# Optimization experiments

Hardware: AMD Instinct MI355X
Metric: run time of the kernel (lower is better)

## Reference

```python
import jax, jax.numpy as jnp
import numpy as np

TEMPERATURE = 11.313708498984761  # sqrt(128)


def setup_inputs() -> dict:
    key = jax.random.key(0)
    kq, kk, kv = jax.random.split(key, 3)
    b, n, m, d, dv = 16, 2048, 2048, 128, 128
    return {
        "queries": jax.random.normal(kq, (b, n, d), dtype=jnp.float32),
        "keys": jax.random.normal(kk, (b, m, d), dtype=jnp.float32),
        "values": jax.random.normal(kv, (b, m, dv), dtype=jnp.float32),
    }


def reference(queries, keys, values):
    # scores: [b, n, m]
    scores = jnp.einsum('bnd,bmd->bnm', queries, keys) / TEMPERATURE
    attn = jax.nn.softmax(scores, axis=2)
    # out: [b, n, d']
    return jnp.einsum('bnm,bmd->bnd', attn, values)
```

## Files before the change

### kernel.cpp

```cpp
#include <hip/hip_runtime.h>


#define BATCH 16
#define SEQ   2048
#define DIM   128
#define NT    (SEQ / 64)

typedef short bf16x8 __attribute__((ext_vector_type(8)));
typedef float f32x16 __attribute__((ext_vector_type(16)));

static __device__ __forceinline__ unsigned pk2(float lo, float hi) {
  union { float f; unsigned u; } a, b;
  a.f = lo; b.f = hi;
  return ((b.u + 0x8000u) & 0xffff0000u) | ((a.u + 0x8000u) >> 16);
}
static __device__ __forceinline__ float fast_exp2(float x) {
#if __has_builtin(__builtin_amdgcn_exp2f)
  return __builtin_amdgcn_exp2f(x);
#else
  return exp2f(x);
#endif
}

typedef __attribute__((address_space(1))) const unsigned int g_u32;
typedef __attribute__((address_space(3))) unsigned int l_u32;
static __device__ __forceinline__ void gl2lds16(const unsigned short* g, unsigned short* l) {
  __builtin_amdgcn_global_load_lds((g_u32*)g, (l_u32*)l, 16, 0, 0);
}

__global__ __launch_bounds__(256)
void prep_kernel(const float* __restrict__ K, const float* __restrict__ V,
                 unsigned short* __restrict__ Kb, unsigned short* __restrict__ Vt,
                 float scale) {
  const int bx = blockIdx.x, tid = threadIdx.x;
  if (bx < 2048) {
    size_t idx = (size_t)bx * 256 + tid;
    const float4* kf = (const float4*)K;
    float4 a = kf[idx * 2], c = kf[idx * 2 + 1];
    uint4 o;
    o.x = pk2(a.x * scale, a.y * scale);
    o.y = pk2(a.z * scale, a.w * scale);
    o.z = pk2(c.x * scale, c.y * scale);
    o.w = pk2(c.z * scale, c.w * scale);
    ((uint4*)Kb)[idx] = o;
  } else {
    __shared__ float tile[128][33];
    const int vb = bx - 2048;
    const int b = vb >> 6, r = vb & 63;
    const int m0 = (r & 15) * 128, d0 = (r >> 4) * 32;
    const int c = tid & 7, mr = tid >> 3;
    const float* src = V + ((size_t)(b * SEQ) + m0) * DIM + d0;
#pragma unroll
    for (int it = 0; it < 4; ++it) {
      int m = it * 32 + mr;
      float4 x = *(const float4*)(src + (size_t)m * DIM + c * 4);
      tile[m][c * 4 + 0] = x.x; tile[m][c * 4 + 1] = x.y;
      tile[m][c * 4 + 2] = x.z; tile[m][c * 4 + 3] = x.w;
    }
    __syncthreads();
    const int dr = tid >> 3, s = tid & 7;
    unsigned short* dst = Vt + ((size_t)(b * DIM) + d0 + dr) * SEQ + m0;
#pragma unroll
    for (int it = 0; it < 2; ++it) {
      int slot = it * 8 + s;
      uint4 o;
      o.x = pk2(tile[slot * 8 + 0][dr], tile[slot * 8 + 1][dr]);
      o.y = pk2(tile[slot * 8 + 2][dr], tile[slot * 8 + 3][dr]);
      o.z = pk2(tile[slot * 8 + 4][dr], tile[slot * 8 + 5][dr]);
      o.w = pk2(tile[slot * 8 + 6][dr], tile[slot * 8 + 7][dr]);
      *(uint4*)(dst + slot * 8) = o;
    }
  }
}


__global__ __launch_bounds__(256, 2)
void attn_kernel(const float* __restrict__ Qf,
                 const unsigned short* __restrict__ Kb,
                 const unsigned short* __restrict__ Vtb,
                 float* __restrict__ out) {
  __shared__ __align__(1024) unsigned char smem[65536];
  unsigned short* sm16 = (unsigned short*)smem;

  const int tid  = threadIdx.x;
  const int wv   = tid >> 6;
  const int w_q  = wv & 1;
  const int w_m  = wv >> 1;
  const int lane = tid & 63;
  const int l31  = lane & 31;
  const int q2   = lane >> 5;
  const int b    = blockIdx.x;
  const int q0   = blockIdx.y * 64 + w_q * 32;

  const unsigned short* kb = Kb  + (size_t)b * SEQ * DIM;
  const unsigned short* vb = Vtb + (size_t)b * SEQ * DIM;

  bf16x8 aq[8];
  {
    const float* qp = Qf + ((size_t)(b * SEQ) + q0 + l31) * DIM + q2 * 8;
#pragma unroll
    for (int c = 0; c < 8; ++c) {
      float4 x = *(const float4*)(qp + c * 16);
      float4 y = *(const float4*)(qp + c * 16 + 4);
      union { unsigned i[4]; bf16x8 v; } u;
      u.i[0] = pk2(x.x, x.y); u.i[1] = pk2(x.z, x.w);
      u.i[2] = pk2(y.x, y.y); u.i[3] = pk2(y.z, y.w);
      aq[c] = u.v;
    }
  }

  unsigned kgo[4], vgo[4];
#pragma unroll
  for (int i = 0; i < 4; ++i) {
    int ch = wv * 4 + i;
    int krow = ch * 4 + (lane >> 4);
    kgo[i] = (unsigned)(krow * 128) + ((((lane & 15) << 4) ^ ((krow & 15) << 4)) >> 1);
    int vrow = ch * 8 + (lane >> 3);
    vgo[i] = (unsigned)(vrow * 2048) + ((((lane & 7) << 4) ^ ((vrow & 7) << 4)) >> 1);
  }

  const int kro = ((w_m * 32 + l31) << 8) + ((q2 << 4) ^ ((l31 & 15) << 4));
  const int vro = (l31 << 7) + (((w_m << 6) + (q2 << 4)) ^ ((l31 & 7) << 4));

  f32x16 oacc[4];
#pragma unroll
  for (int t = 0; t < 4; ++t)
#pragma unroll
    for (int i = 0; i < 16; ++i) oacc[t][i] = 0.0f;
  float ls[4] = {0.0f, 0.0f, 0.0f, 0.0f};

#define STAGE(TK, BUF) do {                                                  \
    const unsigned short* kt_b = kb + ((size_t)(TK) << 13);                  \
    const unsigned short* vt_b = vb + ((TK) << 6);                           \
    unsigned short* kd = sm16 + (((BUF) + wv * 4096) >> 1);                  \
    unsigned short* vd = sm16 + ((32768 + (BUF) + wv * 4096) >> 1);          \
    _Pragma("unroll")                                                        \
    for (int i = 0; i < 4; ++i) gl2lds16(kt_b + kgo[i], kd + i * 512);       \
    _Pragma("unroll")                                                        \
    for (int i = 0; i < 4; ++i) gl2lds16(vt_b + vgo[i], vd + i * 512);       \
  } while (0)

  STAGE(0, 0);

  for (int kt = 0; kt < NT; ++kt) {
    const int cur = (kt & 1) << 14;
    asm volatile("s_waitcnt vmcnt(4)" ::: "memory");
    __builtin_amdgcn_s_barrier();
    __builtin_amdgcn_sched_barrier(0);

    const unsigned char* kB = smem + cur;
    const unsigned char* vB = smem + 32768 + cur;

    f32x16 se, so;
#pragma unroll
    for (int i = 0; i < 16; ++i) { se[i] = 0.0f; so[i] = 0.0f; }
    __builtin_amdgcn_s_setprio(1);
#pragma unroll
    for (int c = 0; c < 4; ++c) {
      bf16x8 b0 = *(const bf16x8*)(kB + (kro ^ ((2 * c) << 5)));
      se = __builtin_amdgcn_mfma_f32_32x32x16_bf16(b0, aq[2 * c], se, 0, 0, 0);
      bf16x8 b1 = *(const bf16x8*)(kB + (kro ^ ((2 * c + 1) << 5)));
      so = __builtin_amdgcn_mfma_f32_32x32x16_bf16(b1, aq[2 * c + 1], so, 0, 0, 0);
    }
    __builtin_amdgcn_s_setprio(0);
    __builtin_amdgcn_sched_barrier(0);

    STAGE((kt + 1) & (NT - 1), 16384 - cur);
    __builtin_amdgcn_sched_barrier(0);

    float p[16];
#pragma unroll
    for (int i = 0; i < 16; ++i) p[i] = fast_exp2(se[i] + so[i]);
#pragma unroll
    for (int i = 0; i < 4; ++i) {
      ls[0] += p[4 * i + 0]; ls[1] += p[4 * i + 1];
      ls[2] += p[4 * i + 2]; ls[3] += p[4 * i + 3];
    }

    unsigned d0, d1, d2, d3, d4, d5, d6, d7;
    asm("v_cvt_pk_bf16_f32 %0, %1, %2" : "=v"(d0) : "v"(p[0]),  "v"(p[1]));
    asm("v_cvt_pk_bf16_f32 %0, %1, %2" : "=v"(d1) : "v"(p[2]),  "v"(p[3]));
    asm("v_cvt_pk_bf16_f32 %0, %1, %2" : "=v"(d2) : "v"(p[4]),  "v"(p[5]));
    asm("v_cvt_pk_bf16_f32 %0, %1, %2" : "=v"(d3) : "v"(p[6]),  "v"(p[7]));
    asm("v_cvt_pk_bf16_f32 %0, %1, %2" : "=v"(d4) : "v"(p[8]),  "v"(p[9]));
    asm("v_cvt_pk_bf16_f32 %0, %1, %2" : "=v"(d5) : "v"(p[10]), "v"(p[11]));
    asm("v_cvt_pk_bf16_f32 %0, %1, %2" : "=v"(d6) : "v"(p[12]), "v"(p[13]));
    asm("v_cvt_pk_bf16_f32 %0, %1, %2" : "=v"(d7) : "v"(p[14]), "v"(p[15]));
    asm("v_permlane32_swap_b32 %0, %1" : "+v"(d0), "+v"(d2));
    asm("v_permlane32_swap_b32 %0, %1" : "+v"(d1), "+v"(d3));
    asm("v_permlane32_swap_b32 %0, %1" : "+v"(d4), "+v"(d6));
    asm("v_permlane32_swap_b32 %0, %1" : "+v"(d5), "+v"(d7));
    union { unsigned u[4]; bf16x8 v; } pu0, pu1;
    pu0.u[0] = d0; pu0.u[1] = d1; pu0.u[2] = d2; pu0.u[3] = d3;
    pu1.u[0] = d4; pu1.u[1] = d5; pu1.u[2] = d6; pu1.u[3] = d7;

    asm volatile("s_waitcnt vmcnt(8)" ::: "memory");
    __builtin_amdgcn_s_barrier();
    __builtin_amdgcn_sched_barrier(0);

    __builtin_amdgcn_s_setprio(1);
#pragma unroll
    for (int t = 0; t < 4; ++t) {
      bf16x8 bv0 = *(const bf16x8*)(vB + t * 4096 + vro);
      oacc[t] = __builtin_amdgcn_mfma_f32_32x32x16_bf16(pu0.v, bv0, oacc[t], 0, 0, 0);
      bf16x8 bv1 = *(const bf16x8*)(vB + t * 4096 + (vro ^ 32));
      oacc[t] = __builtin_amdgcn_mfma_f32_32x32x16_bf16(pu1.v, bv1, oacc[t], 0, 0, 0);
    }
    __builtin_amdgcn_s_setprio(0);
    __builtin_amdgcn_sched_barrier(0);
  }
#undef STAGE

  float lsum = (ls[0] + ls[1]) + (ls[2] + ls[3]);
  lsum += __shfl_xor(lsum, 32, 64);

  __syncthreads();
  float* cb  = (float*)smem;
  float* cbL = (float*)(smem + 32768);
  if (w_m == 1) {
    float* my = cb + w_q * 4096;
#pragma unroll
    for (int t = 0; t < 4; ++t)
#pragma unroll
      for (int r = 0; r < 16; ++r)
        my[(t * 16 + r) * 64 + lane] = oacc[t][r];
  }
  cbL[w_m * 64 + w_q * 32 + l31] = lsum;
  __syncthreads();
  if (w_m == 0) {
    const float* pr = cb + w_q * 4096;
    float linv[16];
#pragma unroll
    for (int r = 0; r < 16; ++r) {
      int qr = (r & 3) + ((r >> 2) << 3) + (q2 << 2);
      linv[r] = 1.0f / (cbL[w_q * 32 + qr] + cbL[64 + w_q * 32 + qr]);
    }
    float* ob = out + ((size_t)(b * SEQ) + q0) * DIM;
#pragma unroll
    for (int t = 0; t < 4; ++t)
#pragma unroll
      for (int r = 0; r < 16; ++r) {
        int qr = (r & 3) + ((r >> 2) << 3) + (q2 << 2);
        ob[(size_t)qr * DIM + t * 32 + l31] = (oacc[t][r] + pr[(t * 16 + r) * 64 + lane]) * linv[r];
      }
  }
}

extern "C" void kernel_launch(void* const* d_in, const int* in_sizes, int n_in,
                              void* d_out, int out_size, void* d_ws, size_t ws_size,
                              hipStream_t stream) {
  const float* Q = (const float*)d_in[0];
  const float* K = (const float*)d_in[1];
  const float* V = (const float*)d_in[2];
  float* out = (float*)d_out;

  const size_t elems = (size_t)BATCH * SEQ * DIM;
  unsigned short* Kb = (unsigned short*)d_ws;
  unsigned short* Vt = Kb + elems;

  const double TEMPERATURE = 11.313708498984761;
  const float scale = (float)(1.4426950408889634 / TEMPERATURE);

  prep_kernel<<<3072, 256, 0, stream>>>(K, V, Kb, Vt, scale);
  attn_kernel<<<dim3(BATCH, SEQ / 64), 256, 0, stream>>>(Q, Kb, Vt, out);
}
```

Measured before the change: 132.6 us.

## Triple-buffer K tiles and prefetch K two iterations ahead

Splits K and V staging so K tiles use a three-slot ring buffer and are prefetched two iterations ahead, while V stays double-buffered one ahead. LDS grows from 64KB to 80KB and wait counts are adjusted. The intent is to hide global load latency for the QK^T stage more fully. With two blocks per CU requested, the larger LDS footprint may limit occupancy.

```diff
diff --git a/kernel.cpp b/kernel.cpp
--- a/kernel.cpp
+++ b/kernel.cpp
@@ -79,7 +79,7 @@
                  const unsigned short* __restrict__ Kb,
                  const unsigned short* __restrict__ Vtb,
                  float* __restrict__ out) {
-  __shared__ __align__(1024) unsigned char smem[65536];
+  __shared__ __align__(1024) unsigned char smem[81920];
   unsigned short* sm16 = (unsigned short*)smem;
 
   const int tid  = threadIdx.x;
@@ -129,27 +129,34 @@
     for (int i = 0; i < 16; ++i) oacc[t][i] = 0.0f;
   float ls[4] = {0.0f, 0.0f, 0.0f, 0.0f};
 
-#define STAGE(TK, BUF) do {                                                  \
+#define STAGE_K(TK, KOFF) do {                                               \
     const unsigned short* kt_b = kb + ((size_t)(TK) << 13);                  \
-    const unsigned short* vt_b = vb + ((TK) << 6);                           \
-    unsigned short* kd = sm16 + (((BUF) + wv * 4096) >> 1);                  \
-    unsigned short* vd = sm16 + ((32768 + (BUF) + wv * 4096) >> 1);          \
+    unsigned short* kd = sm16 + (((KOFF) + wv * 4096) >> 1);                 \
     _Pragma("unroll")                                                        \
     for (int i = 0; i < 4; ++i) gl2lds16(kt_b + kgo[i], kd + i * 512);       \
+  } while (0)
+#define STAGE_V(TV, VOFF) do {                                               \
+    const unsigned short* vt_b = vb + ((TV) << 6);                           \
+    unsigned short* vd = sm16 + (((VOFF) + wv * 4096) >> 1);                 \
     _Pragma("unroll")                                                        \
     for (int i = 0; i < 4; ++i) gl2lds16(vt_b + vgo[i], vd + i * 512);       \
   } while (0)
 
-  STAGE(0, 0);
+  STAGE_K(0, 0);
+  STAGE_V(0, 49152);
+  STAGE_K(1, 16384);
+
+  int kcur = 0;
+  int kstg = 32768;
+  int vcur = 0;
 
   for (int kt = 0; kt < NT; ++kt) {
-    const int cur = (kt & 1) << 14;
-    asm volatile("s_waitcnt vmcnt(4)" ::: "memory");
+    asm volatile("s_waitcnt vmcnt(8)" ::: "memory");
     __builtin_amdgcn_s_barrier();
     __builtin_amdgcn_sched_barrier(0);
 
-    const unsigned char* kB = smem + cur;
-    const unsigned char* vB = smem + 32768 + cur;
+    const unsigned char* kB = smem + kcur;
+    const unsigned char* vB = smem + 49152 + vcur;
 
     f32x16 se, so;
 #pragma unroll
@@ -165,7 +172,8 @@
     __builtin_amdgcn_s_setprio(0);
     __builtin_amdgcn_sched_barrier(0);
 
-    STAGE((kt + 1) & (NT - 1), 16384 - cur);
+    STAGE_K((kt + 2) & (NT - 1), kstg);
+    STAGE_V((kt + 1) & (NT - 1), 49152 + (vcur ^ 16384));
     __builtin_amdgcn_sched_barrier(0);
 
     float p[16];
@@ -208,8 +216,13 @@
     }
     __builtin_amdgcn_s_setprio(0);
     __builtin_amdgcn_sched_barrier(0);
-  }
-#undef STAGE
+
+    kcur = (kcur == 32768) ? 0 : kcur + 16384;
+    kstg = (kstg == 32768) ? 0 : kstg + 16384;
+    vcur ^= 16384;
+  }
+#undef STAGE_K
+#undef STAGE_V
 
   float lsum = (ls[0] + ls[1]) + (ls[2] + ls[3]);
   lsum += __shfl_xor(lsum, 32, 64);
```

Result: no change. 134.2 us (+1.3%).
